# Optimization experiments

Measured on AMD Instinct MI355X. Metric: run time of the kernel, lower is better.

The kernel has to match this reference:

```python
import jax, jax.numpy as jnp
import numpy as np

N = 100000      # nodes
E = 1600000     # edges (before self-loops)
C_IN, C_HID, HEADS, C_OUT = 128, 32, 4, 64
NEG_SLOPE = 0.2  # PyG GATConv default


def setup_inputs() -> dict:
    key = jax.random.key(0)
    ks = jax.random.split(key, 10)
    x = jax.random.normal(ks[0], (N, C_IN), dtype=jnp.float32)
    edge_index = jax.random.randint(ks[1], (2, E), 0, N)
    g1 = 1.0 / np.sqrt(C_IN)
    g2 = 1.0 / np.sqrt(C_HID * HEADS)
    return {
        "x": x,
        "edge_index": edge_index,
        "W1": jax.random.normal(ks[2], (C_IN, HEADS * C_HID), jnp.float32) * g1,
        "att_src1": jax.random.normal(ks[3], (HEADS, C_HID), jnp.float32) * g2,
        "att_dst1": jax.random.normal(ks[4], (HEADS, C_HID), jnp.float32) * g2,
        "b1": jnp.zeros((HEADS * C_HID,), jnp.float32),
        "W2": jax.random.normal(ks[5], (HEADS * C_HID, 1 * C_OUT), jnp.float32) * g2,
        "att_src2": jax.random.normal(ks[6], (1, C_OUT), jnp.float32) * (1.0 / np.sqrt(C_OUT)),
        "att_dst2": jax.random.normal(ks[7], (1, C_OUT), jnp.float32) * (1.0 / np.sqrt(C_OUT)),
        "b2": jnp.zeros((C_OUT,), jnp.float32),
    }


def _gat_layer(x, src, dst, W, att_src, att_dst, bias):
    """PyG GATConv (v1): xp = xW; alpha_e = softmax_dst(leaky_relu(a_s[src]+a_d[dst]))."""
    H, C = att_src.shape
    xp = (x @ W).reshape(-1, H, C)                      # [N, H, C]
    a_src = jnp.einsum('nhc,hc->nh', xp, att_src)        # [N, H]
    a_dst = jnp.einsum('nhc,hc->nh', xp, att_dst)        # [N, H]
    logits = jax.nn.leaky_relu(a_src[src] + a_dst[dst], NEG_SLOPE)  # [E, H]
    m = jax.lax.stop_gradient(jax.ops.segment_max(logits, dst, num_segments=N))
    e = jnp.exp(logits - m[dst])                         # [E, H]
    denom = jax.ops.segment_sum(e, dst, num_segments=N)  # [N, H]
    alpha = e / denom[dst]                               # [E, H]
    msg = xp[src] * alpha[..., None]                     # [E, H, C]
    out = jax.ops.segment_sum(msg, dst, num_segments=N)  # [N, H, C]
    return out.reshape(-1, H * C) + bias


def reference(x, edge_index, W1, att_src1, att_dst1, b1, W2, att_src2, att_dst2, b2):
    # add_self_loops=True (PyG default)
    loops = jnp.arange(N, dtype=edge_index.dtype)
    src = jnp.concatenate([edge_index[0], loops])
    dst = jnp.concatenate([edge_index[1], loops])
    h = _gat_layer(x, src, dst, W1, att_src1, att_dst1, b1)
    h = jax.nn.elu(h)                                    # Dropout is identity in eval
    out = _gat_layer(h, src, dst, W2, att_src2, att_dst2, b2)
    return out
```

## Files before the change

kernel.cpp:

```cpp
#include <hip/hip_runtime.h>
#include <hip/hip_bf16.h>
#include <math.h>

#define NN 100000
#define NE 1600000
#define ET (NE + NN)
#define CIN 128
#define H1 4
#define C1 32
#define HC1 128
#define C2 64
#define NEG 0.2f
#define NB1 196
#define SBLK 256
#define ECHUNK ((NE + SBLK - 1) / SBLK)
#define BCAP 12288
#define WN 13
#define CURN (512 * WN)

typedef __attribute__((ext_vector_type(8))) short short8v;
typedef __attribute__((ext_vector_type(4))) float f32x4;

__device__ __forceinline__ float bfu2f(unsigned short u) {
  union { unsigned u; float f; } c; c.u = ((unsigned)u) << 16; return c.f;
}
__device__ __forceinline__ float bflo(unsigned v) {
  union { unsigned u; float f; } c; c.u = v << 16; return c.f;
}
__device__ __forceinline__ float bfhi(unsigned v) {
  union { unsigned u; float f; } c; c.u = v & 0xffff0000u; return c.f;
}
__device__ __forceinline__ unsigned short f2bfu(float f) {
  union { __hip_bfloat16 b; unsigned short u; } c; c.b = __float2bfloat16(f); return c.u;
}

__global__ void k_detect(const unsigned short* __restrict__ x, int* __restrict__ flag) {
  __shared__ int cnt;
  if (threadIdx.x == 0) cnt = 0;
  __syncthreads();
  int bad = 0;
  for (int i = threadIdx.x; i < 2048; i += 256) {
    unsigned short u = x[i];
    int ex = (u >> 7) & 0xFF;
    bool ok = ((u & 0x7FFF) == 0) || (ex >= 90 && ex <= 140);
    if (!ok) bad++;
  }
  atomicAdd(&cnt, bad);
  __syncthreads();
  if (threadIdx.x == 0) *flag = (cnt * 10 < 2048) ? 1 : 0;
}

__global__ void k_params(const void* __restrict__ W1, const void* __restrict__ W2,
                         const void* as1, const void* ad1, const void* b1,
                         const void* as2, const void* ad2, const void* b2,
                         unsigned short* __restrict__ W1b, unsigned short* __restrict__ W2b,
                         float* pAS1, float* pAD1, float* b1f,
                         float* pAS2, float* pAD2, float* b2f,
                         const int* __restrict__ flag) {
  int g = blockIdx.x * 256 + threadIdx.x;
  int isbf = *flag;
  auto cv = [&](const void* p, int idx) -> float {
    return isbf ? bfu2f(((const unsigned short*)p)[idx]) : ((const float*)p)[idx];
  };
  if (g < CIN * HC1) {
    W1b[g] = isbf ? ((const unsigned short*)W1)[g] : f2bfu(((const float*)W1)[g]);
  } else if (g < CIN * HC1 + HC1 * C2) {
    int i = g - CIN * HC1;
    W2b[i] = isbf ? ((const unsigned short*)W2)[i] : f2bfu(((const float*)W2)[i]);
  } else {
    int i = g - (CIN * HC1 + HC1 * C2);
    if (i < HC1) { pAS1[i] = cv(as1, i); pAD1[i] = cv(ad1, i); b1f[i] = cv(b1, i); }
    else if (i < HC1 + C2) {
      int j = i - HC1;
      pAS2[j] = cv(as2, j); pAD2[j] = cv(ad2, j); b2f[j] = cv(b2, j);
    }
  }
}

__global__ __launch_bounds__(256) void k_histo(
    const int* __restrict__ dst, int* __restrict__ gcnt) {
  __shared__ int hist[NB1];
  for (int b = threadIdx.x; b < NB1; b += 256) hist[b] = 0;
  __syncthreads();
  int e0 = blockIdx.x * ECHUNK;
  int e1 = min(e0 + ECHUNK, NE);
  for (int e = e0 + threadIdx.x; e < e1; e += 256)
    atomicAdd(&hist[dst[e] >> 9], 1);
  __syncthreads();
  for (int b = threadIdx.x; b < NB1; b += 256)
    gcnt[b * SBLK + blockIdx.x] = hist[b];
}

__global__ void k_histscan(int* __restrict__ gcnt, int* __restrict__ bucketReal) {
  __shared__ int sm[SBLK];
  int b = blockIdx.x;
  int t = threadIdx.x;
  int v = gcnt[b * SBLK + t];
  sm[t] = v;
  __syncthreads();
  for (int off = 1; off < SBLK; off <<= 1) {
    int tmp = (t >= off) ? sm[t - off] : 0;
    __syncthreads();
    sm[t] += tmp;
    __syncthreads();
  }
  gcnt[b * SBLK + t] = sm[t] - v;
  if (t == SBLK - 1) bucketReal[b] = sm[SBLK - 1];
}

__global__ void k_base(const int* __restrict__ bucketReal, int* __restrict__ sBase,
                       int* __restrict__ rowptr2) {
  __shared__ int sm[256];
  int t = threadIdx.x;
  int v = (t < NB1) ? bucketReal[t] : 0;
  sm[t] = v;
  __syncthreads();
  for (int off = 1; off < 256; off <<= 1) {
    int tmp = (t >= off) ? sm[t - off] : 0;
    __syncthreads();
    sm[t] += tmp;
    __syncthreads();
  }
  if (t < NB1) sBase[t] = sm[t] - v;
  if (t == 0) rowptr2[(size_t)NN * WN] = ET;
}

__global__ __launch_bounds__(256) void k_scatter(
    const int* __restrict__ src, const int* __restrict__ dst,
    const int* __restrict__ gcnt, const int* __restrict__ sBase,
    unsigned* __restrict__ staging) {
  __shared__ int lcur[NB1];
  for (int b = threadIdx.x; b < NB1; b += 256)
    lcur[b] = sBase[b] + gcnt[b * SBLK + blockIdx.x];
  __syncthreads();
  int e0 = blockIdx.x * ECHUNK;
  int e1 = min(e0 + ECHUNK, NE);
  for (int e = e0 + threadIdx.x; e < e1; e += 256) {
    int s = src[e], d = dst[e];
    int pos = atomicAdd(&lcur[d >> 9], 1);
    staging[pos] = (unsigned)s | ((unsigned)(d & 511) << 17);
  }
}

__global__ __launch_bounds__(256) void k_bucket2(
    const unsigned* __restrict__ staging, const int* __restrict__ sBase,
    const int* __restrict__ bucketReal, int* __restrict__ rowptr2,
    int* __restrict__ col) {
  __shared__ int lhist[CURN];
  __shared__ int lcol[BCAP];
  __shared__ int ps[256];
  int b = blockIdx.x;
  int t = threadIdx.x;
  int n0 = b << 9;
  int nc = min(512, NN - n0);
  int sb = sBase[b];
  int realE = bucketReal[b];
  int regionStart = sb + n0;
  int total = realE + nc;
#pragma unroll
  for (int q = 0; q < CURN / 256; ++q) lhist[t + q * 256] = 0;
  __syncthreads();
  for (int i = t; i < realE; i += 256) {
    unsigned p = staging[sb + i];
    int d = (int)(p >> 17);
    int w = (int)((p & 0x1FFFFu) >> 13);
    atomicAdd(&lhist[d * WN + w], 1);
  }
  for (int i = t; i < nc; i += 256)
    atomicAdd(&lhist[i * WN + ((n0 + i) >> 13)], 1);
  __syncthreads();
  constexpr int CHUNK = CURN / 256;
  int vals[CHUNK];
  int run = 0;
#pragma unroll
  for (int i = 0; i < CHUNK; ++i) { vals[i] = lhist[t * CHUNK + i]; run += vals[i]; }
  ps[t] = run;
  __syncthreads();
  for (int off = 1; off < 256; off <<= 1) {
    int tmp = (t >= off) ? ps[t - off] : 0;
    __syncthreads();
    ps[t] += tmp;
    __syncthreads();
  }
  int base = ps[t] - run;
#pragma unroll
  for (int i = 0; i < CHUNK; ++i) { lhist[t * CHUNK + i] = base; base += vals[i]; }
  __syncthreads();
  for (int i = t; i < nc * WN; i += 256)
    rowptr2[(size_t)n0 * WN + i] = regionStart + lhist[i];
  __syncthreads();
  for (int i = t; i < nc; i += 256) {
    int r = atomicAdd(&lhist[i * WN + ((n0 + i) >> 13)], 1);
    if (r < BCAP) lcol[r] = n0 + i;
    else col[regionStart + r] = n0 + i;
  }
  for (int i = t; i < realE; i += 256) {
    unsigned p = staging[sb + i];
    int d = (int)(p >> 17);
    int s = (int)(p & 0x1FFFFu);
    int r = atomicAdd(&lhist[d * WN + (s >> 13)], 1);
    if (r < BCAP) lcol[r] = s;
    else col[regionStart + r] = s;
  }
  __syncthreads();
  int lim = min(total, BCAP);
  for (int i = t; i < lim; i += 256)
    col[regionStart + i] = lcol[i];
}

template<int NT, int H, bool MAYBE_F32>
__global__ __launch_bounds__(256) void k_gemm_mfma(
    const void* __restrict__ Araw, const unsigned short* __restrict__ W,
    unsigned short* __restrict__ Cb, const float* __restrict__ attS,
    const float* __restrict__ attD, float* __restrict__ ns,
    float* __restrict__ nd, int M, const int* __restrict__ flag) {
  constexpr int NC = NT * 16;
  __shared__ __align__(16) unsigned short lds[NC * 128];
  int t = threadIdx.x;
#pragma unroll
  for (int r = 0; r < (128 * NC) / (256 * 8); ++r) {
    int f = (t + r * 256) * 8;
    int k = f / NC;
    int n0 = f - k * NC;
    short8v v = *(const short8v*)(W + k * NC + n0);
#pragma unroll
    for (int j = 0; j < 8; ++j) {
      int n = n0 + j;
      lds[n * 128 + (((k >> 3) ^ (n & 7)) << 3) + (k & 7)] = ((const unsigned short*)&v)[j];
    }
  }
  __syncthreads();
  int wave = t >> 6, lane = t & 63;
  int m0 = (blockIdx.x * 4 + wave) * 32;
  if (m0 >= M) return;
  int isbf = MAYBE_F32 ? *flag : 1;
  f32x4 acc[2][NT];
#pragma unroll
  for (int mt = 0; mt < 2; ++mt)
#pragma unroll
    for (int nt = 0; nt < NT; ++nt) acc[mt][nt] = (f32x4)(0.f);
  int r0 = m0 + (lane & 15);
  int koff = (lane >> 4) << 3;
#pragma unroll
  for (int ks = 0; ks < 4; ++ks) {
    short8v af0, af1;
    if (isbf) {
      const unsigned short* A = (const unsigned short*)Araw;
      af0 = *(const short8v*)(A + (size_t)r0 * 128 + koff + ks * 32);
      af1 = *(const short8v*)(A + (size_t)(r0 + 16) * 128 + koff + ks * 32);
    } else {
      const float* A = (const float*)Araw;
      const float* p0 = A + (size_t)r0 * 128 + koff + ks * 32;
      const float* p1 = A + (size_t)(r0 + 16) * 128 + koff + ks * 32;
      float4 u0 = *(const float4*)p0, u1 = *(const float4*)(p0 + 4);
      float4 v0 = *(const float4*)p1, v1 = *(const float4*)(p1 + 4);
      unsigned short* a0 = (unsigned short*)&af0;
      unsigned short* a1 = (unsigned short*)&af1;
      a0[0] = f2bfu(u0.x); a0[1] = f2bfu(u0.y); a0[2] = f2bfu(u0.z); a0[3] = f2bfu(u0.w);
      a0[4] = f2bfu(u1.x); a0[5] = f2bfu(u1.y); a0[6] = f2bfu(u1.z); a0[7] = f2bfu(u1.w);
      a1[0] = f2bfu(v0.x); a1[1] = f2bfu(v0.y); a1[2] = f2bfu(v0.z); a1[3] = f2bfu(v0.w);
      a1[4] = f2bfu(v1.x); a1[5] = f2bfu(v1.y); a1[6] = f2bfu(v1.z); a1[7] = f2bfu(v1.w);
    }
#pragma unroll
    for (int nt = 0; nt < NT; ++nt) {
      int n = nt * 16 + (lane & 15);
      int chunk = ks * 4 + (lane >> 4);
      short8v bf = *(const short8v*)&lds[n * 128 + ((chunk ^ (n & 7)) << 3)];
      acc[0][nt] = __builtin_amdgcn_mfma_f32_16x16x32_bf16(af0, bf, acc[0][nt], 0, 0, 0);
      acc[1][nt] = __builtin_amdgcn_mfma_f32_16x16x32_bf16(af1, bf, acc[1][nt], 0, 0, 0);
    }
  }
  constexpr int NPH = NT / H;
#pragma unroll
  for (int mt = 0; mt < 2; ++mt) {
    int mb = m0 + mt * 16;
#pragma unroll
    for (int nt = 0; nt < NT; ++nt)
#pragma unroll
      for (int r = 0; r < 4; ++r) {
        int row = ((lane >> 4) << 2) + r;
        Cb[(size_t)(mb + row) * NC + nt * 16 + (lane & 15)] = f2bfu(acc[mt][nt][r]);
      }
#pragma unroll
    for (int r = 0; r < 4; ++r) {
      int row = mb + ((lane >> 4) << 2) + r;
#pragma unroll
      for (int h = 0; h < H; ++h) {
        float ps = 0.f, pd = 0.f;
#pragma unroll
        for (int q = 0; q < NPH; ++q) {
          int nt = h * NPH + q;
          int ch = nt * 16 + (lane & 15);
          ps = fmaf(acc[mt][nt][r], attS[ch], ps);
          pd = fmaf(acc[mt][nt][r], attD[ch], pd);
        }
#pragma unroll
        for (int off = 8; off; off >>= 1) {
          ps += __shfl_xor(ps, off);
          pd += __shfl_xor(pd, off);
        }
        if ((lane & 15) == 0) { ns[row * H + h] = ps; nd[row * H + h] = pd; }
      }
    }
  }
}

template<int CPL>
__device__ __forceinline__ void accum(float w, const unsigned short* p, float* acc) {
#pragma unroll
  for (int q = 0; q < CPL / 8; ++q) {
    uint4 v = *(const uint4*)(p + q * 8);
    acc[q * 8 + 0] = fmaf(w, bflo(v.x), acc[q * 8 + 0]);
    acc[q * 8 + 1] = fmaf(w, bfhi(v.x), acc[q * 8 + 1]);
    acc[q * 8 + 2] = fmaf(w, bflo(v.y), acc[q * 8 + 2]);
    acc[q * 8 + 3] = fmaf(w, bfhi(v.y), acc[q * 8 + 3]);
    acc[q * 8 + 4] = fmaf(w, bflo(v.z), acc[q * 8 + 4]);
    acc[q * 8 + 5] = fmaf(w, bfhi(v.z), acc[q * 8 + 5]);
    acc[q * 8 + 6] = fmaf(w, bflo(v.w), acc[q * 8 + 6]);
    acc[q * 8 + 7] = fmaf(w, bfhi(v.w), acc[q * 8 + 7]);
  }
}

template<int H, int C, int LPE, bool DOELU, bool FINAL>
__global__ __launch_bounds__(256) void k_agg(
    const int* __restrict__ rowptr2, const int* __restrict__ col,
    const float* __restrict__ ns, const float* __restrict__ nd,
    const unsigned short* __restrict__ xp, const float* __restrict__ bias,
    void* __restrict__ outp, const int* __restrict__ flag) {
  constexpr int HC = H * C;
  constexpr int CPL = HC / LPE;
  constexpr int EPW = 64 / LPE;
  int wave = threadIdx.x >> 6;
  int lane = threadIdx.x & 63;
  int n = blockIdx.x * 4 + wave;
  if (n >= NN) return;
  int rs = rowptr2[(size_t)n * WN];
  int deg = rowptr2[(size_t)n * WN + WN] - rs;
  int le = lane & (LPE - 1);
  int eg = lane / LPE;
  int ch0 = le * CPL;
  int h = (H == 1) ? 0 : (ch0 / C);
  float ndv = nd[n * H + h];
  const unsigned short* xpc = xp + ch0;
  float den = 0.f;
  float acc[CPL];
#pragma unroll
  for (int c = 0; c < CPL; ++c) acc[c] = 0.f;
  int j = eg;
  for (; j + EPW < deg; j += 2 * EPW) {
    int s0 = col[rs + j], s1 = col[rs + j + EPW];
    float l0 = ns[s0 * H + h] + ndv, l1 = ns[s1 * H + h] + ndv;
    l0 = l0 >= 0.f ? l0 : NEG * l0;
    l1 = l1 >= 0.f ? l1 : NEG * l1;
    float w0 = __expf(l0), w1 = __expf(l1);
    den += w0 + w1;
    const unsigned short* p0 = xpc + (size_t)s0 * HC;
    const unsigned short* p1 = xpc + (size_t)s1 * HC;
    accum<CPL>(w0, p0, acc);
    accum<CPL>(w1, p1, acc);
  }
  if (j < deg) {
    int s = col[rs + j];
    float l = ns[s * H + h] + ndv;
    l = l >= 0.f ? l : NEG * l;
    float w = __expf(l);
    den += w;
    accum<CPL>(w, xpc + (size_t)s * HC, acc);
  }
#pragma unroll
  for (int off = 32; off >= LPE; off >>= 1) {
    den += __shfl_xor(den, off);
#pragma unroll
    for (int c = 0; c < CPL; ++c) acc[c] += __shfl_xor(acc[c], off);
  }
  if (eg != 0) return;
  float inv = 1.f / den;
  float o[CPL];
#pragma unroll
  for (int c = 0; c < CPL; ++c) {
    o[c] = acc[c] * inv + bias[ch0 + c];
    if (DOELU) o[c] = o[c] > 0.f ? o[c] : __expf(o[c]) - 1.f;
  }
  if (FINAL && !*flag) {
    float* op = (float*)outp + (size_t)n * HC + ch0;
#pragma unroll
    for (int q = 0; q < CPL / 4; ++q)
      *(float4*)(op + q * 4) = make_float4(o[q * 4], o[q * 4 + 1], o[q * 4 + 2], o[q * 4 + 3]);
  } else {
    unsigned short* op = (unsigned short*)outp + (size_t)n * HC + ch0;
#pragma unroll
    for (int q = 0; q < CPL / 8; ++q) {
      uint4 pk;
      pk.x = (unsigned)f2bfu(o[q * 8 + 0]) | ((unsigned)f2bfu(o[q * 8 + 1]) << 16);
      pk.y = (unsigned)f2bfu(o[q * 8 + 2]) | ((unsigned)f2bfu(o[q * 8 + 3]) << 16);
      pk.z = (unsigned)f2bfu(o[q * 8 + 4]) | ((unsigned)f2bfu(o[q * 8 + 5]) << 16);
      pk.w = (unsigned)f2bfu(o[q * 8 + 6]) | ((unsigned)f2bfu(o[q * 8 + 7]) << 16);
      *(uint4*)(op + q * 8) = pk;
    }
  }
}

extern "C" void kernel_launch(void* const* d_in, const int* in_sizes, int n_in,
                              void* d_out, int out_size, void* d_ws, size_t ws_size,
                              hipStream_t stream) {
  const void* x  = d_in[0];
  const int* ei  = (const int*)d_in[1];
  const void* W1 = d_in[2];
  const void* as1 = d_in[3];
  const void* ad1 = d_in[4];
  const void* b1 = d_in[5];
  const void* W2 = d_in[6];
  const void* as2 = d_in[7];
  const void* ad2 = d_in[8];
  const void* b2 = d_in[9];
  const int* srcs = ei;
  const int* dsts = ei + NE;

  char* w = (char*)d_ws;
  auto alloc = [&](size_t bytes) {
    char* p = w;
    w += (bytes + 255) & ~(size_t)255;
    return p;
  };
  int* flag   = (int*)alloc(4);
  unsigned short* hb  = (unsigned short*)alloc((size_t)NN * HC1 * 2);
  unsigned short* W1b = (unsigned short*)alloc((size_t)CIN * HC1 * 2);
  unsigned short* W2b = (unsigned short*)alloc((size_t)HC1 * C2 * 2);
  unsigned short* xp1 = (unsigned short*)alloc((size_t)NN * HC1 * 2);
  float* nAS1 = (float*)alloc((size_t)NN * H1 * 4);
  float* nAD1 = (float*)alloc((size_t)NN * H1 * 4);
  float* nAS2 = (float*)alloc((size_t)NN * 4);
  float* nAD2 = (float*)alloc((size_t)NN * 4);
  float* pAS1 = (float*)alloc((size_t)H1 * C1 * 4);
  float* pAD1 = (float*)alloc((size_t)H1 * C1 * 4);
  float* b1f  = (float*)alloc((size_t)HC1 * 4);
  float* pAS2 = (float*)alloc((size_t)C2 * 4);
  float* pAD2 = (float*)alloc((size_t)C2 * 4);
  float* b2f  = (float*)alloc((size_t)C2 * 4);
  int* rowptr2 = (int*)alloc(((size_t)NN * WN + 1) * 4);
  int* gcnt   = (int*)alloc((size_t)NB1 * SBLK * 4);
  int* bucketReal = (int*)alloc((size_t)NB1 * 4);
  int* sBase  = (int*)alloc((size_t)NB1 * 4);
  int* colx   = (int*)alloc((size_t)ET * 4);
  unsigned* staging = (unsigned*)alloc((size_t)NE * 4);
  unsigned short* xp2 = xp1;

  k_detect<<<1, 256, 0, stream>>>((const unsigned short*)x, flag);
  k_params<<<(CIN * HC1 + HC1 * C2 + HC1 + C2 + 255) / 256, 256, 0, stream>>>(
      W1, W2, as1, ad1, b1, as2, ad2, b2,
      W1b, W2b, pAS1, pAD1, b1f, pAS2, pAD2, b2f, flag);

  k_histo<<<SBLK, 256, 0, stream>>>(dsts, gcnt);
  k_histscan<<<NB1, SBLK, 0, stream>>>(gcnt, bucketReal);
  k_base<<<1, 256, 0, stream>>>(bucketReal, sBase, rowptr2);
  k_scatter<<<SBLK, 256, 0, stream>>>(srcs, dsts, gcnt, sBase, staging);
  k_bucket2<<<NB1, 256, 0, stream>>>(staging, sBase, bucketReal, rowptr2, colx);

  int gb = (NN + 127) / 128;
  k_gemm_mfma<8, H1, true><<<gb, 256, 0, stream>>>(
      x, W1b, xp1, pAS1, pAD1, nAS1, nAD1, NN, flag);
  k_agg<H1, C1, 8, true, false><<<(NN + 3) / 4, 256, 0, stream>>>(
      rowptr2, colx, nAS1, nAD1, xp1, b1f, hb, flag);

  k_gemm_mfma<4, 1, false><<<gb, 256, 0, stream>>>(
      hb, W2b, xp2, pAS2, pAD2, nAS2, nAD2, NN, flag);
  k_agg<1, C2, 8, false, true><<<(NN + 3) / 4, 256, 0, stream>>>(
      rowptr2, colx, nAS2, nAD2, xp2, b2f, d_out, flag);
}
```

Measured before the change: 232.2 us.

## Store layer-1 features head-major and split aggregation per head; simplify CSR build

The first GEMM now writes projected features and attention scores in head-major layout, so each head's features form a compact 12.8 MB table. The layer-1 aggregation is split into per-head blocks, interleaved so the four heads of nearby node groups run close together, to improve cache locality of the random neighbour gathers. The bucketed CSR construction drops its 13-way source-window sub-sorting (rowptr2 with WN windows) and becomes a plain per-node CSR, which cuts shared-memory histogram work but loses the source-locality ordering of neighbour lists. Each layer-1 edge's column index and score are now read four times, once per head.

New measurement: 313.8 us. +35.1%, slower.

```diff
diff --git a/kernel.cpp b/kernel.cpp
--- a/kernel.cpp
+++ b/kernel.cpp
@@ -15,8 +15,6 @@
 #define SBLK 256
 #define ECHUNK ((NE + SBLK - 1) / SBLK)
 #define BCAP 12288
-#define WN 13
-#define CURN (512 * WN)
 
 typedef __attribute__((ext_vector_type(8))) short short8v;
 typedef __attribute__((ext_vector_type(4))) float f32x4;
@@ -109,7 +107,7 @@
 }
 
 __global__ void k_base(const int* __restrict__ bucketReal, int* __restrict__ sBase,
-                       int* __restrict__ rowptr2) {
+                       int* __restrict__ rowptr) {
   __shared__ int sm[256];
   int t = threadIdx.x;
   int v = (t < NB1) ? bucketReal[t] : 0;
@@ -122,7 +120,7 @@
     __syncthreads();
   }
   if (t < NB1) sBase[t] = sm[t] - v;
-  if (t == 0) rowptr2[(size_t)NN * WN] = ET;
+  if (t == 0) rowptr[NN] = ET;
 }
 
 __global__ __launch_bounds__(256) void k_scatter(
@@ -142,11 +140,11 @@
   }
 }
 
-__global__ __launch_bounds__(256) void k_bucket2(
+__global__ __launch_bounds__(256) void k_bucket(
     const unsigned* __restrict__ staging, const int* __restrict__ sBase,
-    const int* __restrict__ bucketReal, int* __restrict__ rowptr2,
+    const int* __restrict__ bucketReal, int* __restrict__ rowptr,
     int* __restrict__ col) {
-  __shared__ int lhist[CURN];
+  __shared__ int lhist[512];
   __shared__ int lcol[BCAP];
   __shared__ int ps[256];
   int b = blockIdx.x;
@@ -157,23 +155,14 @@
   int realE = bucketReal[b];
   int regionStart = sb + n0;
   int total = realE + nc;
-#pragma unroll
-  for (int q = 0; q < CURN / 256; ++q) lhist[t + q * 256] = 0;
-  __syncthreads();
-  for (int i = t; i < realE; i += 256) {
-    unsigned p = staging[sb + i];
-    int d = (int)(p >> 17);
-    int w = (int)((p & 0x1FFFFu) >> 13);
-    atomicAdd(&lhist[d * WN + w], 1);
-  }
-  for (int i = t; i < nc; i += 256)
-    atomicAdd(&lhist[i * WN + ((n0 + i) >> 13)], 1);
-  __syncthreads();
-  constexpr int CHUNK = CURN / 256;
-  int vals[CHUNK];
-  int run = 0;
-#pragma unroll
-  for (int i = 0; i < CHUNK; ++i) { vals[i] = lhist[t * CHUNK + i]; run += vals[i]; }
+  lhist[t] = (t < nc) ? 1 : 0;
+  lhist[t + 256] = (t + 256 < nc) ? 1 : 0;
+  __syncthreads();
+  for (int i = t; i < realE; i += 256)
+    atomicAdd(&lhist[staging[sb + i] >> 17], 1);
+  __syncthreads();
+  int v0 = lhist[t * 2], v1 = lhist[t * 2 + 1];
+  int run = v0 + v1;
   ps[t] = run;
   __syncthreads();
   for (int off = 1; off < 256; off <<= 1) {
@@ -183,24 +172,23 @@
     __syncthreads();
   }
   int base = ps[t] - run;
-#pragma unroll
-  for (int i = 0; i < CHUNK; ++i) { lhist[t * CHUNK + i] = base; base += vals[i]; }
-  __syncthreads();
-  for (int i = t; i < nc * WN; i += 256)
-    rowptr2[(size_t)n0 * WN + i] = regionStart + lhist[i];
+  lhist[t * 2] = base;
+  lhist[t * 2 + 1] = base + v0;
+  __syncthreads();
+  for (int i = t; i < nc; i += 256)
+    rowptr[n0 + i] = regionStart + lhist[i];
   __syncthreads();
   for (int i = t; i < nc; i += 256) {
-    int r = atomicAdd(&lhist[i * WN + ((n0 + i) >> 13)], 1);
+    int r = atomicAdd(&lhist[i], 1);
     if (r < BCAP) lcol[r] = n0 + i;
     else col[regionStart + r] = n0 + i;
   }
   for (int i = t; i < realE; i += 256) {
     unsigned p = staging[sb + i];
-    int d = (int)(p >> 17);
-    int s = (int)(p & 0x1FFFFu);
-    int r = atomicAdd(&lhist[d * WN + (s >> 13)], 1);
-    if (r < BCAP) lcol[r] = s;
-    else col[regionStart + r] = s;
+    int r = atomicAdd(&lhist[p >> 17], 1);
+    int sv = (int)(p & 0x1FFFFu);
+    if (r < BCAP) lcol[r] = sv;
+    else col[regionStart + r] = sv;
   }
   __syncthreads();
   int lim = min(total, BCAP);
@@ -208,13 +196,14 @@
     col[regionStart + i] = lcol[i];
 }
 
-template<int NT, int H, bool MAYBE_F32>
+template<int NT, int H, bool MAYBE_F32, bool HEADMAJOR>
 __global__ __launch_bounds__(256) void k_gemm_mfma(
     const void* __restrict__ Araw, const unsigned short* __restrict__ W,
     unsigned short* __restrict__ Cb, const float* __restrict__ attS,
     const float* __restrict__ attD, float* __restrict__ ns,
     float* __restrict__ nd, int M, const int* __restrict__ flag) {
   constexpr int NC = NT * 16;
+  constexpr int C = NC / H;
   __shared__ __align__(16) unsigned short lds[NC * 128];
   int t = threadIdx.x;
 #pragma unroll
@@ -278,8 +267,14 @@
     for (int nt = 0; nt < NT; ++nt)
 #pragma unroll
       for (int r = 0; r < 4; ++r) {
-        int row = ((lane >> 4) << 2) + r;
-        Cb[(size_t)(mb + row) * NC + nt * 16 + (lane & 15)] = f2bfu(acc[mt][nt][r]);
+        int row = mb + ((lane >> 4) << 2) + r;
+        int ch = nt * 16 + (lane & 15);
+        if (HEADMAJOR) {
+          int h = ch / C, c = ch % C;
+          Cb[(size_t)h * M * C + (size_t)row * C + c] = f2bfu(acc[mt][nt][r]);
+        } else {
+          Cb[(size_t)row * NC + ch] = f2bfu(acc[mt][nt][r]);
+        }
       }
 #pragma unroll
     for (int r = 0; r < 4; ++r) {
@@ -299,48 +294,109 @@
           ps += __shfl_xor(ps, off);
           pd += __shfl_xor(pd, off);
         }
-        if ((lane & 15) == 0) { ns[row * H + h] = ps; nd[row * H + h] = pd; }
+        if ((lane & 15) == 0) {
+          if (HEADMAJOR) { ns[(size_t)h * M + row] = ps; nd[(size_t)h * M + row] = pd; }
+          else { ns[row * H + h] = ps; nd[row * H + h] = pd; }
+        }
       }
     }
   }
 }
 
-template<int CPL>
-__device__ __forceinline__ void accum(float w, const unsigned short* p, float* acc) {
-#pragma unroll
-  for (int q = 0; q < CPL / 8; ++q) {
-    uint4 v = *(const uint4*)(p + q * 8);
-    acc[q * 8 + 0] = fmaf(w, bflo(v.x), acc[q * 8 + 0]);
-    acc[q * 8 + 1] = fmaf(w, bfhi(v.x), acc[q * 8 + 1]);
-    acc[q * 8 + 2] = fmaf(w, bflo(v.y), acc[q * 8 + 2]);
-    acc[q * 8 + 3] = fmaf(w, bfhi(v.y), acc[q * 8 + 3]);
-    acc[q * 8 + 4] = fmaf(w, bflo(v.z), acc[q * 8 + 4]);
-    acc[q * 8 + 5] = fmaf(w, bfhi(v.z), acc[q * 8 + 5]);
-    acc[q * 8 + 6] = fmaf(w, bflo(v.w), acc[q * 8 + 6]);
-    acc[q * 8 + 7] = fmaf(w, bfhi(v.w), acc[q * 8 + 7]);
-  }
-}
-
-template<int H, int C, int LPE, bool DOELU, bool FINAL>
-__global__ __launch_bounds__(256) void k_agg(
-    const int* __restrict__ rowptr2, const int* __restrict__ col,
+__global__ __launch_bounds__(256) void k_agg1h(
+    const int* __restrict__ rowptr, const int* __restrict__ col,
+    const float* __restrict__ nsh, const float* __restrict__ ndh,
+    const unsigned short* __restrict__ xph, const float* __restrict__ bias,
+    unsigned short* __restrict__ hb) {
+  constexpr int LPE = 4, EPW = 16, CPL = 8;
+  int wave = threadIdx.x >> 6;
+  int lane = threadIdx.x & 63;
+  int b7 = blockIdx.x & 7;
+  int h = b7 >> 1;
+  int i = ((blockIdx.x >> 3) << 1) + (b7 & 1);
+  int n = i * 4 + wave;
+  if (n >= NN) return;
+  int rs = rowptr[n];
+  int deg = rowptr[n + 1] - rs;
+  int le = lane & (LPE - 1);
+  int eg = lane >> 2;
+  int ch0 = le * CPL;
+  const float* nsp = nsh + (size_t)h * NN;
+  float ndv = ndh[(size_t)h * NN + n];
+  const unsigned short* xpb = xph + (size_t)h * NN * C1 + ch0;
+  float den = 0.f;
+  float acc[CPL];
+#pragma unroll
+  for (int c = 0; c < CPL; ++c) acc[c] = 0.f;
+  int j = eg;
+  for (; j + EPW < deg; j += 2 * EPW) {
+    int s0 = col[rs + j], s1 = col[rs + j + EPW];
+    float l0 = nsp[s0] + ndv, l1 = nsp[s1] + ndv;
+    l0 = l0 >= 0.f ? l0 : NEG * l0;
+    l1 = l1 >= 0.f ? l1 : NEG * l1;
+    float w0 = __expf(l0), w1 = __expf(l1);
+    den += w0 + w1;
+    uint4 v0 = *(const uint4*)(xpb + (size_t)s0 * C1);
+    uint4 v1 = *(const uint4*)(xpb + (size_t)s1 * C1);
+    acc[0] = fmaf(w0, bflo(v0.x), acc[0]); acc[1] = fmaf(w0, bfhi(v0.x), acc[1]);
+    acc[2] = fmaf(w0, bflo(v0.y), acc[2]); acc[3] = fmaf(w0, bfhi(v0.y), acc[3]);
+    acc[4] = fmaf(w0, bflo(v0.z), acc[4]); acc[5] = fmaf(w0, bfhi(v0.z), acc[5]);
+    acc[6] = fmaf(w0, bflo(v0.w), acc[6]); acc[7] = fmaf(w0, bfhi(v0.w), acc[7]);
+    acc[0] = fmaf(w1, bflo(v1.x), acc[0]); acc[1] = fmaf(w1, bfhi(v1.x), acc[1]);
+    acc[2] = fmaf(w1, bflo(v1.y), acc[2]); acc[3] = fmaf(w1, bfhi(v1.y), acc[3]);
+    acc[4] = fmaf(w1, bflo(v1.z), acc[4]); acc[5] = fmaf(w1, bfhi(v1.z), acc[5]);
+    acc[6] = fmaf(w1, bflo(v1.w), acc[6]); acc[7] = fmaf(w1, bfhi(v1.w), acc[7]);
+  }
+  if (j < deg) {
+    int s = col[rs + j];
+    float l = nsp[s] + ndv;
+    l = l >= 0.f ? l : NEG * l;
+    float w = __expf(l);
+    den += w;
+    uint4 v = *(const uint4*)(xpb + (size_t)s * C1);
+    acc[0] = fmaf(w, bflo(v.x), acc[0]); acc[1] = fmaf(w, bfhi(v.x), acc[1]);
+    acc[2] = fmaf(w, bflo(v.y), acc[2]); acc[3] = fmaf(w, bfhi(v.y), acc[3]);
+    acc[4] = fmaf(w, bflo(v.z), acc[4]); acc[5] = fmaf(w, bfhi(v.z), acc[5]);
+    acc[6] = fmaf(w, bflo(v.w), acc[6]); acc[7] = fmaf(w, bfhi(v.w), acc[7]);
+  }
+#pragma unroll
+  for (int off = 32; off >= LPE; off >>= 1) {
+    den += __shfl_xor(den, off);
+#pragma unroll
+    for (int c = 0; c < CPL; ++c) acc[c] += __shfl_xor(acc[c], off);
+  }
+  if (eg != 0) return;
+  float inv = 1.f / den;
+  float o[CPL];
+#pragma unroll
+  for (int c = 0; c < CPL; ++c) {
+    o[c] = acc[c] * inv + bias[h * C1 + ch0 + c];
+    o[c] = o[c] > 0.f ? o[c] : __expf(o[c]) - 1.f;
+  }
+  uint4 pk;
+  pk.x = (unsigned)f2bfu(o[0]) | ((unsigned)f2bfu(o[1]) << 16);
+  pk.y = (unsigned)f2bfu(o[2]) | ((unsigned)f2bfu(o[3]) << 16);
+  pk.z = (unsigned)f2bfu(o[4]) | ((unsigned)f2bfu(o[5]) << 16);
+  pk.w = (unsigned)f2bfu(o[6]) | ((unsigned)f2bfu(o[7]) << 16);
+  *(uint4*)(hb + (size_t)n * HC1 + h * C1 + ch0) = pk;
+}
+
+__global__ __launch_bounds__(256) void k_agg2(
+    const int* __restrict__ rowptr, const int* __restrict__ col,
     const float* __restrict__ ns, const float* __restrict__ nd,
     const unsigned short* __restrict__ xp, const float* __restrict__ bias,
     void* __restrict__ outp, const int* __restrict__ flag) {
-  constexpr int HC = H * C;
-  constexpr int CPL = HC / LPE;
-  constexpr int EPW = 64 / LPE;
+  constexpr int HC = C2, LPE = 8, CPL = 8, EPW = 8;
   int wave = threadIdx.x >> 6;
   int lane = threadIdx.x & 63;
   int n = blockIdx.x * 4 + wave;
   if (n >= NN) return;
-  int rs = rowptr2[(size_t)n * WN];
-  int deg = rowptr2[(size_t)n * WN + WN] - rs;
+  int rs = rowptr[n];
+  int deg = rowptr[n + 1] - rs;
   int le = lane & (LPE - 1);
   int eg = lane / LPE;
   int ch0 = le * CPL;
-  int h = (H == 1) ? 0 : (ch0 / C);
-  float ndv = nd[n * H + h];
+  float ndv = nd[n];
   const unsigned short* xpc = xp + ch0;
   float den = 0.f;
   float acc[CPL];
@@ -349,23 +405,33 @@
   int j = eg;
   for (; j + EPW < deg; j += 2 * EPW) {
     int s0 = col[rs + j], s1 = col[rs + j + EPW];
-    float l0 = ns[s0 * H + h] + ndv, l1 = ns[s1 * H + h] + ndv;
+    float l0 = ns[s0] + ndv, l1 = ns[s1] + ndv;
     l0 = l0 >= 0.f ? l0 : NEG * l0;
     l1 = l1 >= 0.f ? l1 : NEG * l1;
     float w0 = __expf(l0), w1 = __expf(l1);
     den += w0 + w1;
-    const unsigned short* p0 = xpc + (size_t)s0 * HC;
-    const unsigned short* p1 = xpc + (size_t)s1 * HC;
-    accum<CPL>(w0, p0, acc);
-    accum<CPL>(w1, p1, acc);
+    uint4 v0 = *(const uint4*)(xpc + (size_t)s0 * HC);
+    uint4 v1 = *(const uint4*)(xpc + (size_t)s1 * HC);
+    acc[0] = fmaf(w0, bflo(v0.x), acc[0]); acc[1] = fmaf(w0, bfhi(v0.x), acc[1]);
+    acc[2] = fmaf(w0, bflo(v0.y), acc[2]); acc[3] = fmaf(w0, bfhi(v0.y), acc[3]);
+    acc[4] = fmaf(w0, bflo(v0.z), acc[4]); acc[5] = fmaf(w0, bfhi(v0.z), acc[5]);
+    acc[6] = fmaf(w0, bflo(v0.w), acc[6]); acc[7] = fmaf(w0, bfhi(v0.w), acc[7]);
+    acc[0] = fmaf(w1, bflo(v1.x), acc[0]); acc[1] = fmaf(w1, bfhi(v1.x), acc[1]);
+    acc[2] = fmaf(w1, bflo(v1.y), acc[2]); acc[3] = fmaf(w1, bfhi(v1.y), acc[3]);
+    acc[4] = fmaf(w1, bflo(v1.z), acc[4]); acc[5] = fmaf(w1, bfhi(v1.z), acc[5]);
+    acc[6] = fmaf(w1, bflo(v1.w), acc[6]); acc[7] = fmaf(w1, bfhi(v1.w), acc[7]);
   }
   if (j < deg) {
     int s = col[rs + j];
-    float l = ns[s * H + h] + ndv;
+    float l = ns[s] + ndv;
     l = l >= 0.f ? l : NEG * l;
     float w = __expf(l);
     den += w;
-    accum<CPL>(w, xpc + (size_t)s * HC, acc);
+    uint4 v = *(const uint4*)(xpc + (size_t)s * HC);
+    acc[0] = fmaf(w, bflo(v.x), acc[0]); acc[1] = fmaf(w, bfhi(v.x), acc[1]);
+    acc[2] = fmaf(w, bflo(v.y), acc[2]); acc[3] = fmaf(w, bfhi(v.y), acc[3]);
+    acc[4] = fmaf(w, bflo(v.z), acc[4]); acc[5] = fmaf(w, bfhi(v.z), acc[5]);
+    acc[6] = fmaf(w, bflo(v.w), acc[6]); acc[7] = fmaf(w, bfhi(v.w), acc[7]);
   }
 #pragma unroll
   for (int off = 32; off >= LPE; off >>= 1) {
@@ -377,26 +443,19 @@
   float inv = 1.f / den;
   float o[CPL];
 #pragma unroll
-  for (int c = 0; c < CPL; ++c) {
-    o[c] = acc[c] * inv + bias[ch0 + c];
-    if (DOELU) o[c] = o[c] > 0.f ? o[c] : __expf(o[c]) - 1.f;
-  }
-  if (FINAL && !*flag) {
+  for (int c = 0; c < CPL; ++c) o[c] = acc[c] * inv + bias[ch0 + c];
+  if (!*flag) {
     float* op = (float*)outp + (size_t)n * HC + ch0;
-#pragma unroll
-    for (int q = 0; q < CPL / 4; ++q)
-      *(float4*)(op + q * 4) = make_float4(o[q * 4], o[q * 4 + 1], o[q * 4 + 2], o[q * 4 + 3]);
+    *(float4*)op = make_float4(o[0], o[1], o[2], o[3]);
+    *(float4*)(op + 4) = make_float4(o[4], o[5], o[6], o[7]);
   } else {
     unsigned short* op = (unsigned short*)outp + (size_t)n * HC + ch0;
-#pragma unroll
-    for (int q = 0; q < CPL / 8; ++q) {
-      uint4 pk;
-      pk.x = (unsigned)f2bfu(o[q * 8 + 0]) | ((unsigned)f2bfu(o[q * 8 + 1]) << 16);
-      pk.y = (unsigned)f2bfu(o[q * 8 + 2]) | ((unsigned)f2bfu(o[q * 8 + 3]) << 16);
-      pk.z = (unsigned)f2bfu(o[q * 8 + 4]) | ((unsigned)f2bfu(o[q * 8 + 5]) << 16);
-      pk.w = (unsigned)f2bfu(o[q * 8 + 6]) | ((unsigned)f2bfu(o[q * 8 + 7]) << 16);
-      *(uint4*)(op + q * 8) = pk;
-    }
+    uint4 pk;
+    pk.x = (unsigned)f2bfu(o[0]) | ((unsigned)f2bfu(o[1]) << 16);
+    pk.y = (unsigned)f2bfu(o[2]) | ((unsigned)f2bfu(o[3]) << 16);
+    pk.z = (unsigned)f2bfu(o[4]) | ((unsigned)f2bfu(o[5]) << 16);
+    pk.w = (unsigned)f2bfu(o[6]) | ((unsigned)f2bfu(o[7]) << 16);
+    *(uint4*)op = pk;
   }
 }
 
@@ -437,7 +496,7 @@
   float* pAS2 = (float*)alloc((size_t)C2 * 4);
   float* pAD2 = (float*)alloc((size_t)C2 * 4);
   float* b2f  = (float*)alloc((size_t)C2 * 4);
-  int* rowptr2 = (int*)alloc(((size_t)NN * WN + 1) * 4);
+  int* rowptr = (int*)alloc((size_t)(NN + 1) * 4);
   int* gcnt   = (int*)alloc((size_t)NB1 * SBLK * 4);
   int* bucketReal = (int*)alloc((size_t)NB1 * 4);
   int* sBase  = (int*)alloc((size_t)NB1 * 4);
@@ -452,18 +511,16 @@
 
   k_histo<<<SBLK, 256, 0, stream>>>(dsts, gcnt);
   k_histscan<<<NB1, SBLK, 0, stream>>>(gcnt, bucketReal);
-  k_base<<<1, 256, 0, stream>>>(bucketReal, sBase, rowptr2);
+  k_base<<<1, 256, 0, stream>>>(bucketReal, sBase, rowptr);
   k_scatter<<<SBLK, 256, 0, stream>>>(srcs, dsts, gcnt, sBase, staging);
-  k_bucket2<<<NB1, 256, 0, stream>>>(staging, sBase, bucketReal, rowptr2, colx);
+  k_bucket<<<NB1, 256, 0, stream>>>(staging, sBase, bucketReal, rowptr, colx);
 
   int gb = (NN + 127) / 128;
-  k_gemm_mfma<8, H1, true><<<gb, 256, 0, stream>>>(
+  k_gemm_mfma<8, H1, true, true><<<gb, 256, 0, stream>>>(
       x, W1b, xp1, pAS1, pAD1, nAS1, nAD1, NN, flag);
-  k_agg<H1, C1, 8, true, false><<<(NN + 3) / 4, 256, 0, stream>>>(
-      rowptr2, colx, nAS1, nAD1, xp1, b1f, hb, flag);
-
-  k_gemm_mfma<4, 1, false><<<gb, 256, 0, stream>>>(
+  k_agg1h<<<12500 * 8, 256, 0, stream>>>(rowptr, colx, nAS1, nAD1, xp1, b1f, hb);
+
+  k_gemm_mfma<4, 1, false, false><<<gb, 256, 0, stream>>>(
       hb, W2b, xp2, pAS2, pAD2, nAS2, nAD2, NN, flag);
-  k_agg<1, C2, 8, false, true><<<(NN + 3) / 4, 256, 0, stream>>>(
-      rowptr2, colx, nAS2, nAD2, xp2, b2f, d_out, flag);
-}
+  k_agg2<<<(NN + 3) / 4, 256, 0, stream>>>(rowptr, colx, nAS2, nAD2, xp2, b2f, d_out, flag);
+}
```

## Replace source-window sorted CSR with plain per-destination CSR and add nontemporal accesses

Applied to the files above, without the earlier changes.

The bucketing kernel no longer sub-sorts each destination's edges into 13 source windows. It builds a simple per-node histogram and a 512-entry scan, so rowptr shrinks from N*13 to N+1 entries and the local histogram from 6656 to 512 ints. This cuts CSR-build work, LDS use and rowptr writes. The cost is that gathers in aggregation are no longer grouped by source range, which may lose L2 locality on xp and ns. Nontemporal loads and stores are also added for edge indices, col and outputs.

New measurement: 252.2 us. 1.09x slower.

```diff
diff --git a/kernel.cpp b/kernel.cpp
--- a/kernel.cpp
+++ b/kernel.cpp
@@ -15,11 +15,10 @@
 #define SBLK 256
 #define ECHUNK ((NE + SBLK - 1) / SBLK)
 #define BCAP 12288
-#define WN 13
-#define CURN (512 * WN)
 
 typedef __attribute__((ext_vector_type(8))) short short8v;
 typedef __attribute__((ext_vector_type(4))) float f32x4;
+typedef __attribute__((ext_vector_type(4))) unsigned int u32x4;
 
 __device__ __forceinline__ float bfu2f(unsigned short u) {
   union { unsigned u; float f; } c; c.u = ((unsigned)u) << 16; return c.f;
@@ -85,7 +84,7 @@
   int e0 = blockIdx.x * ECHUNK;
   int e1 = min(e0 + ECHUNK, NE);
   for (int e = e0 + threadIdx.x; e < e1; e += 256)
-    atomicAdd(&hist[dst[e] >> 9], 1);
+    atomicAdd(&hist[__builtin_nontemporal_load(dst + e) >> 9], 1);
   __syncthreads();
   for (int b = threadIdx.x; b < NB1; b += 256)
     gcnt[b * SBLK + blockIdx.x] = hist[b];
@@ -109,7 +108,7 @@
 }
 
 __global__ void k_base(const int* __restrict__ bucketReal, int* __restrict__ sBase,
-                       int* __restrict__ rowptr2) {
+                       int* __restrict__ rowptr) {
   __shared__ int sm[256];
   int t = threadIdx.x;
   int v = (t < NB1) ? bucketReal[t] : 0;
@@ -122,7 +121,7 @@
     __syncthreads();
   }
   if (t < NB1) sBase[t] = sm[t] - v;
-  if (t == 0) rowptr2[(size_t)NN * WN] = ET;
+  if (t == 0) rowptr[NN] = ET;
 }
 
 __global__ __launch_bounds__(256) void k_scatter(
@@ -136,17 +135,18 @@
   int e0 = blockIdx.x * ECHUNK;
   int e1 = min(e0 + ECHUNK, NE);
   for (int e = e0 + threadIdx.x; e < e1; e += 256) {
-    int s = src[e], d = dst[e];
+    int s = __builtin_nontemporal_load(src + e);
+    int d = __builtin_nontemporal_load(dst + e);
     int pos = atomicAdd(&lcur[d >> 9], 1);
     staging[pos] = (unsigned)s | ((unsigned)(d & 511) << 17);
   }
 }
 
-__global__ __launch_bounds__(256) void k_bucket2(
+__global__ __launch_bounds__(256) void k_bucket(
     const unsigned* __restrict__ staging, const int* __restrict__ sBase,
-    const int* __restrict__ bucketReal, int* __restrict__ rowptr2,
+    const int* __restrict__ bucketReal, int* __restrict__ rowptr,
     int* __restrict__ col) {
-  __shared__ int lhist[CURN];
+  __shared__ int lhist[512];
   __shared__ int lcol[BCAP];
   __shared__ int ps[256];
   int b = blockIdx.x;
@@ -157,55 +157,45 @@
   int realE = bucketReal[b];
   int regionStart = sb + n0;
   int total = realE + nc;
-#pragma unroll
-  for (int q = 0; q < CURN / 256; ++q) lhist[t + q * 256] = 0;
-  __syncthreads();
+  lhist[t] = (t < nc) ? 1 : 0;
+  lhist[t + 256] = (t + 256 < nc) ? 1 : 0;
+  __syncthreads();
+  for (int i = t; i < realE; i += 256)
+    atomicAdd(&lhist[staging[sb + i] >> 17], 1);
+  __syncthreads();
+  int v0 = lhist[t * 2], v1 = lhist[t * 2 + 1];
+  int run = v0 + v1;
+  ps[t] = run;
+  __syncthreads();
+  for (int off = 1; off < 256; off <<= 1) {
+    int tmp = (t >= off) ? ps[t - off] : 0;
+    __syncthreads();
+    ps[t] += tmp;
+    __syncthreads();
+  }
+  int base = ps[t] - run;
+  lhist[t * 2] = base;
+  lhist[t * 2 + 1] = base + v0;
+  __syncthreads();
+  for (int i = t; i < nc; i += 256)
+    rowptr[n0 + i] = regionStart + lhist[i];
+  __syncthreads();
+  for (int i = t; i < nc; i += 256) {
+    int r = atomicAdd(&lhist[i], 1);
+    if (r < BCAP) lcol[r] = n0 + i;
+    else col[regionStart + r] = n0 + i;
+  }
   for (int i = t; i < realE; i += 256) {
     unsigned p = staging[sb + i];
-    int d = (int)(p >> 17);
-    int w = (int)((p & 0x1FFFFu) >> 13);
-    atomicAdd(&lhist[d * WN + w], 1);
-  }
-  for (int i = t; i < nc; i += 256)
-    atomicAdd(&lhist[i * WN + ((n0 + i) >> 13)], 1);
-  __syncthreads();
-  constexpr int CHUNK = CURN / 256;
-  int vals[CHUNK];
-  int run = 0;
-#pragma unroll
-  for (int i = 0; i < CHUNK; ++i) { vals[i] = lhist[t * CHUNK + i]; run += vals[i]; }
-  ps[t] = run;
-  __syncthreads();
-  for (int off = 1; off < 256; off <<= 1) {
-    int tmp = (t >= off) ? ps[t - off] : 0;
-    __syncthreads();
-    ps[t] += tmp;
-    __syncthreads();
-  }
-  int base = ps[t] - run;
-#pragma unroll
-  for (int i = 0; i < CHUNK; ++i) { lhist[t * CHUNK + i] = base; base += vals[i]; }
-  __syncthreads();
-  for (int i = t; i < nc * WN; i += 256)
-    rowptr2[(size_t)n0 * WN + i] = regionStart + lhist[i];
-  __syncthreads();
-  for (int i = t; i < nc; i += 256) {
-    int r = atomicAdd(&lhist[i * WN + ((n0 + i) >> 13)], 1);
-    if (r < BCAP) lcol[r] = n0 + i;
-    else col[regionStart + r] = n0 + i;
-  }
-  for (int i = t; i < realE; i += 256) {
-    unsigned p = staging[sb + i];
-    int d = (int)(p >> 17);
-    int s = (int)(p & 0x1FFFFu);
-    int r = atomicAdd(&lhist[d * WN + (s >> 13)], 1);
-    if (r < BCAP) lcol[r] = s;
-    else col[regionStart + r] = s;
+    int r = atomicAdd(&lhist[p >> 17], 1);
+    int sv = (int)(p & 0x1FFFFu);
+    if (r < BCAP) lcol[r] = sv;
+    else col[regionStart + r] = sv;
   }
   __syncthreads();
   int lim = min(total, BCAP);
   for (int i = t; i < lim; i += 256)
-    col[regionStart + i] = lcol[i];
+    __builtin_nontemporal_store(lcol[i], col + regionStart + i);
 }
 
 template<int NT, int H, bool MAYBE_F32>
@@ -323,7 +313,7 @@
 
 template<int H, int C, int LPE, bool DOELU, bool FINAL>
 __global__ __launch_bounds__(256) void k_agg(
-    const int* __restrict__ rowptr2, const int* __restrict__ col,
+    const int* __restrict__ rowptr, const int* __restrict__ col,
     const float* __restrict__ ns, const float* __restrict__ nd,
     const unsigned short* __restrict__ xp, const float* __restrict__ bias,
     void* __restrict__ outp, const int* __restrict__ flag) {
@@ -334,8 +324,8 @@
   int lane = threadIdx.x & 63;
   int n = blockIdx.x * 4 + wave;
   if (n >= NN) return;
-  int rs = rowptr2[(size_t)n * WN];
-  int deg = rowptr2[(size_t)n * WN + WN] - rs;
+  int rs = rowptr[n];
+  int deg = rowptr[n + 1] - rs;
   int le = lane & (LPE - 1);
   int eg = lane / LPE;
   int ch0 = le * CPL;
@@ -348,7 +338,8 @@
   for (int c = 0; c < CPL; ++c) acc[c] = 0.f;
   int j = eg;
   for (; j + EPW < deg; j += 2 * EPW) {
-    int s0 = col[rs + j], s1 = col[rs + j + EPW];
+    int s0 = __builtin_nontemporal_load(col + rs + j);
+    int s1 = __builtin_nontemporal_load(col + rs + j + EPW);
     float l0 = ns[s0 * H + h] + ndv, l1 = ns[s1 * H + h] + ndv;
     l0 = l0 >= 0.f ? l0 : NEG * l0;
     l1 = l1 >= 0.f ? l1 : NEG * l1;
@@ -360,7 +351,7 @@
     accum<CPL>(w1, p1, acc);
   }
   if (j < deg) {
-    int s = col[rs + j];
+    int s = __builtin_nontemporal_load(col + rs + j);
     float l = ns[s * H + h] + ndv;
     l = l >= 0.f ? l : NEG * l;
     float w = __expf(l);
@@ -384,18 +375,21 @@
   if (FINAL && !*flag) {
     float* op = (float*)outp + (size_t)n * HC + ch0;
 #pragma unroll
-    for (int q = 0; q < CPL / 4; ++q)
-      *(float4*)(op + q * 4) = make_float4(o[q * 4], o[q * 4 + 1], o[q * 4 + 2], o[q * 4 + 3]);
+    for (int q = 0; q < CPL / 4; ++q) {
+      f32x4 fv;
+      fv[0] = o[q * 4]; fv[1] = o[q * 4 + 1]; fv[2] = o[q * 4 + 2]; fv[3] = o[q * 4 + 3];
+      __builtin_nontemporal_store(fv, (f32x4*)(op + q * 4));
+    }
   } else {
     unsigned short* op = (unsigned short*)outp + (size_t)n * HC + ch0;
 #pragma unroll
     for (int q = 0; q < CPL / 8; ++q) {
-      uint4 pk;
-      pk.x = (unsigned)f2bfu(o[q * 8 + 0]) | ((unsigned)f2bfu(o[q * 8 + 1]) << 16);
-      pk.y = (unsigned)f2bfu(o[q * 8 + 2]) | ((unsigned)f2bfu(o[q * 8 + 3]) << 16);
-      pk.z = (unsigned)f2bfu(o[q * 8 + 4]) | ((unsigned)f2bfu(o[q * 8 + 5]) << 16);
-      pk.w = (unsigned)f2bfu(o[q * 8 + 6]) | ((unsigned)f2bfu(o[q * 8 + 7]) << 16);
-      *(uint4*)(op + q * 8) = pk;
+      u32x4 pk;
+      pk[0] = (unsigned)f2bfu(o[q * 8 + 0]) | ((unsigned)f2bfu(o[q * 8 + 1]) << 16);
+      pk[1] = (unsigned)f2bfu(o[q * 8 + 2]) | ((unsigned)f2bfu(o[q * 8 + 3]) << 16);
+      pk[2] = (unsigned)f2bfu(o[q * 8 + 4]) | ((unsigned)f2bfu(o[q * 8 + 5]) << 16);
+      pk[3] = (unsigned)f2bfu(o[q * 8 + 6]) | ((unsigned)f2bfu(o[q * 8 + 7]) << 16);
+      __builtin_nontemporal_store(pk, (u32x4*)(op + q * 8));
     }
   }
 }
@@ -437,7 +431,7 @@
   float* pAS2 = (float*)alloc((size_t)C2 * 4);
   float* pAD2 = (float*)alloc((size_t)C2 * 4);
   float* b2f  = (float*)alloc((size_t)C2 * 4);
-  int* rowptr2 = (int*)alloc(((size_t)NN * WN + 1) * 4);
+  int* rowptr = (int*)alloc((size_t)(NN + 1) * 4);
   int* gcnt   = (int*)alloc((size_t)NB1 * SBLK * 4);
   int* bucketReal = (int*)alloc((size_t)NB1 * 4);
   int* sBase  = (int*)alloc((size_t)NB1 * 4);
@@ -452,18 +446,18 @@
 
   k_histo<<<SBLK, 256, 0, stream>>>(dsts, gcnt);
   k_histscan<<<NB1, SBLK, 0, stream>>>(gcnt, bucketReal);
-  k_base<<<1, 256, 0, stream>>>(bucketReal, sBase, rowptr2);
+  k_base<<<1, 256, 0, stream>>>(bucketReal, sBase, rowptr);
   k_scatter<<<SBLK, 256, 0, stream>>>(srcs, dsts, gcnt, sBase, staging);
-  k_bucket2<<<NB1, 256, 0, stream>>>(staging, sBase, bucketReal, rowptr2, colx);
+  k_bucket<<<NB1, 256, 0, stream>>>(staging, sBase, bucketReal, rowptr, colx);
 
   int gb = (NN + 127) / 128;
   k_gemm_mfma<8, H1, true><<<gb, 256, 0, stream>>>(
       x, W1b, xp1, pAS1, pAD1, nAS1, nAD1, NN, flag);
   k_agg<H1, C1, 8, true, false><<<(NN + 3) / 4, 256, 0, stream>>>(
-      rowptr2, colx, nAS1, nAD1, xp1, b1f, hb, flag);
+      rowptr, colx, nAS1, nAD1, xp1, b1f, hb, flag);
 
   k_gemm_mfma<4, 1, false><<<gb, 256, 0, stream>>>(
       hb, W2b, xp2, pAS2, pAD2, nAS2, nAD2, NN, flag);
   k_agg<1, C2, 8, false, true><<<(NN + 3) / 4, 256, 0, stream>>>(
-      rowptr2, colx, nAS2, nAD2, xp2, b2f, d_out, flag);
-}
+      rowptr, colx, nAS2, nAD2, xp2, b2f, d_out, flag);
+}
```
